# Kernel optimization log

Measured on AMD Instinct MI355X. Metric: run time of the kernel, lower is better.

Reference implementation:

```python
import jax, jax.numpy as jnp
import numpy as np

BS, N, D = 4, 512, 128

def setup_inputs() -> dict:
    key = jax.random.key(0)
    ks = jax.random.split(key, 8)
    s = 1.0 / np.sqrt(D)
    return {
        "x":  jax.random.normal(ks[0], (BS, N, D), dtype=jnp.float32),
        "Wq": jax.random.normal(ks[1], (D, D), dtype=jnp.float32) * s,
        "bq": jax.random.normal(ks[2], (D,), dtype=jnp.float32) * s,
        "Wk": jax.random.normal(ks[3], (D, D), dtype=jnp.float32) * s,
        "bk": jax.random.normal(ks[4], (D,), dtype=jnp.float32) * s,
        "Wv": jax.random.normal(ks[5], (D, D), dtype=jnp.float32) * s,
        "bv": jax.random.normal(ks[6], (D,), dtype=jnp.float32) * s,
        "pos_bias": jax.random.normal(ks[7], (N, N), dtype=jnp.float32) * 0.1,
    }

def reference(x, Wq, bq, Wk, bk, Wv, bv, pos_bias):
    # Linear projections (torch Linear: x @ W^T + b)
    q = jax.nn.sigmoid(jnp.einsum('bnd,ed->bne', x, Wq) + bq)   # [B,N,D]
    k = jnp.einsum('bnd,ed->bne', x, Wk) + bk                   # [B,N,D]
    v = jnp.einsum('bnd,ed->bne', x, Wv) + bv                   # [B,N,D]
    # scores[b,t,j,d] = k[b,j,d] + pos_bias[t,j]  (O(n^2 d) intermediate)
    s = k[:, None, :, :] + pos_bias[None, :, :, None]           # [B,N,N,D]
    m = jnp.max(s, axis=2, keepdims=True)                       # stabilizer
    e = jnp.exp(s - m)                                          # [B,N,N,D]
    num = jnp.einsum('btjd,bjd->btd', e, v)                     # [B,N,D]
    den = jnp.sum(e, axis=2)                                    # [B,N,D]
    return q * (num / den)
```

## Files before the change

### kernel.cpp

```cpp
#include <hip/hip_runtime.h>

#define BATCH 4
#define SEQ   512
#define DIM   128

typedef _Float16 half8 __attribute__((ext_vector_type(8)));
typedef _Float16 half4 __attribute__((ext_vector_type(4)));
typedef float    f32x4 __attribute__((ext_vector_type(4)));

__global__ __launch_bounds__(256) void k_prep(
    const float* __restrict__ x, const float* __restrict__ pos,
    const float* __restrict__ Wq, const float* __restrict__ Wk,
    const float* __restrict__ Wv,
    _Float16* __restrict__ x_h, _Float16* __restrict__ ep_h,
    _Float16* __restrict__ wq_h, _Float16* __restrict__ wk_h,
    _Float16* __restrict__ wv_h)
{
    const int blk = blockIdx.x;
    const int tid = threadIdx.x;
    if (blk < 128) {
        const int i = (blk * 256 + tid) * 8;
        const float4 p0 = *(const float4*)(x + i);
        const float4 p1 = *(const float4*)(x + i + 4);
        half8 h;
        h[0]=(_Float16)p0.x; h[1]=(_Float16)p0.y; h[2]=(_Float16)p0.z; h[3]=(_Float16)p0.w;
        h[4]=(_Float16)p1.x; h[5]=(_Float16)p1.y; h[6]=(_Float16)p1.z; h[7]=(_Float16)p1.w;
        *(half8*)(x_h + i) = h;
    } else if (blk < 256) {
        const int i = ((blk - 128) * 256 + tid) * 8;
        const float4 p0 = *(const float4*)(pos + i);
        const float4 p1 = *(const float4*)(pos + i + 4);
        half8 h;
        h[0]=(_Float16)__expf(p0.x); h[1]=(_Float16)__expf(p0.y);
        h[2]=(_Float16)__expf(p0.z); h[3]=(_Float16)__expf(p0.w);
        h[4]=(_Float16)__expf(p1.x); h[5]=(_Float16)__expf(p1.y);
        h[6]=(_Float16)__expf(p1.z); h[7]=(_Float16)__expf(p1.w);
        *(half8*)(ep_h + i) = h;
    } else {
        const int r = blk - 256;
        const float* src = (r < 8) ? Wq : ((r < 16) ? Wk : Wv);
        _Float16* dst    = (r < 8) ? wq_h : ((r < 16) ? wk_h : wv_h);
        const int i = ((r & 7) * 256 + tid) * 8;
        const float4 p0 = *(const float4*)(src + i);
        const float4 p1 = *(const float4*)(src + i + 4);
        half8 h;
        h[0]=(_Float16)p0.x; h[1]=(_Float16)p0.y; h[2]=(_Float16)p0.z; h[3]=(_Float16)p0.w;
        h[4]=(_Float16)p1.x; h[5]=(_Float16)p1.y; h[6]=(_Float16)p1.z; h[7]=(_Float16)p1.w;
        *(half8*)(dst + i) = h;
    }
}

__global__ __launch_bounds__(256) void k_proj(
    const _Float16* __restrict__ x_h,
    const _Float16* __restrict__ wq_h, const float* __restrict__ bq,
    const _Float16* __restrict__ wk_h, const float* __restrict__ bk,
    const _Float16* __restrict__ wv_h, const float* __restrict__ bv,
    float* __restrict__ qout, _Float16* __restrict__ ekk)
{
    const int tid  = threadIdx.x;
    const int lane = tid & 63;
    const int wave = tid >> 6;
    const int l15  = lane & 15;
    const int quad = lane >> 4;

    const int n0 = (blockIdx.x & 7) * 16;
    const int m0 = (blockIdx.x >> 3) * 64 + wave * 16;

    const _Float16* xa = x_h  + (m0 + l15) * DIM + quad * 8;
    const _Float16* wq = wq_h + (n0 + l15) * DIM + quad * 8;
    const _Float16* wk = wk_h + (n0 + l15) * DIM + quad * 8;
    const _Float16* wv = wv_h + (n0 + l15) * DIM + quad * 8;

    f32x4 aq = {0.f, 0.f, 0.f, 0.f};
    f32x4 ak = {0.f, 0.f, 0.f, 0.f};
    f32x4 av = {0.f, 0.f, 0.f, 0.f};

#pragma unroll
    for (int ks = 0; ks < 4; ++ks) {
        const half8 a  = *(const half8*)(xa + ks * 32);
        const half8 b0 = *(const half8*)(wq + ks * 32);
        const half8 b1 = *(const half8*)(wk + ks * 32);
        const half8 b2 = *(const half8*)(wv + ks * 32);
        aq = __builtin_amdgcn_mfma_f32_16x16x32_f16(a, b0, aq, 0, 0, 0);
        ak = __builtin_amdgcn_mfma_f32_16x16x32_f16(a, b1, ak, 0, 0, 0);
        av = __builtin_amdgcn_mfma_f32_16x16x32_f16(a, b2, av, 0, 0, 0);
    }

    const int c   = n0 + l15;
    const float bqv = bq[c];
    const float bkv = bk[c];
    const float bvv = bv[c];

    const int mrow = m0 + quad * 4;
    const int b    = mrow >> 9;
    const int tok  = mrow & 511;

    half4 eh, evh;
#pragma unroll
    for (int r = 0; r < 4; ++r) {
        const float e  = __expf(ak[r] + bkv);
        const float vv = av[r] + bvv;
        const float qv = 1.f / (1.f + __expf(-(aq[r] + bqv)));
        eh[r]  = (_Float16)e;
        evh[r] = (_Float16)(e * vv);
        qout[(b * SEQ + tok + r) * DIM + c] = qv;
    }
    *(half4*)(ekk + ((b * 256) + 2 * c + 0) * SEQ + tok) = eh;
    *(half4*)(ekk + ((b * 256) + 2 * c + 1) * SEQ + tok) = evh;
}

__global__ __launch_bounds__(256) void k_aft(
    const _Float16* __restrict__ ekk,
    const _Float16* __restrict__ ep_h,
    const float* __restrict__ qout,
    float* __restrict__ out)
{
    const int tid  = threadIdx.x;
    const int lane = tid & 63;
    const int wave = tid >> 6;
    const int l15  = lane & 15;
    const int quad = lane >> 4;
    const int wm   = wave & 1;
    const int wn   = wave >> 1;

    const int b  = blockIdx.x >> 6;
    const int m0 = (((blockIdx.x >> 3) & 7) * 32) + wm * 16;
    const int t0 = ((blockIdx.x & 7) * 64) + wn * 32;

    const _Float16* arow  = ekk  + ((b * 256) + m0 + l15) * SEQ + quad * 8;
    const _Float16* brow0 = ep_h + (t0 + l15) * SEQ + quad * 8;
    const _Float16* brow1 = brow0 + 16 * SEQ;

    f32x4 acc0 = {0.f, 0.f, 0.f, 0.f};
    f32x4 acc1 = {0.f, 0.f, 0.f, 0.f};

#pragma unroll
    for (int ks = 0; ks < 16; ++ks) {
        const half8 a  = *(const half8*)(arow  + ks * 32);
        const half8 b0 = *(const half8*)(brow0 + ks * 32);
        const half8 b1 = *(const half8*)(brow1 + ks * 32);
        acc0 = __builtin_amdgcn_mfma_f32_16x16x32_f16(a, b0, acc0, 0, 0, 0);
        acc1 = __builtin_amdgcn_mfma_f32_16x16x32_f16(a, b1, acc1, 0, 0, 0);
    }

    const int d0 = (m0 + quad * 4) >> 1;
#pragma unroll
    for (int i = 0; i < 2; ++i) {
        const f32x4 acc = i ? acc1 : acc0;
        const int t = t0 + i * 16 + l15;
        const float2 qv = *(const float2*)(qout + ((b * SEQ) + t) * DIM + d0);
        float2 o;
        o.x = qv.x * acc[1] / acc[0];
        o.y = qv.y * acc[3] / acc[2];
        *(float2*)(out + ((b * SEQ) + t) * DIM + d0) = o;
    }
}

extern "C" void kernel_launch(void* const* d_in, const int* in_sizes, int n_in,
                              void* d_out, int out_size, void* d_ws, size_t ws_size,
                              hipStream_t stream) {
    const float* x   = (const float*)d_in[0];
    const float* Wq  = (const float*)d_in[1];
    const float* bq  = (const float*)d_in[2];
    const float* Wk  = (const float*)d_in[3];
    const float* bk  = (const float*)d_in[4];
    const float* Wv  = (const float*)d_in[5];
    const float* bv  = (const float*)d_in[6];
    const float* pos = (const float*)d_in[7];

    float* outp = (float*)d_out;
    char*  ws   = (char*)d_ws;

    _Float16* x_h  = (_Float16*)(ws);
    _Float16* ep_h = (_Float16*)(ws + (512 << 10));
    _Float16* ekk  = (_Float16*)(ws + (1024 << 10));
    _Float16* wq_h = (_Float16*)(ws + (2048 << 10));
    _Float16* wk_h = (_Float16*)(ws + (2080 << 10));
    _Float16* wv_h = (_Float16*)(ws + (2112 << 10));
    float*    qout = (float*)   (ws + (2144 << 10));

    k_prep<<<280, 256, 0, stream>>>(x, pos, Wq, Wk, Wv, x_h, ep_h, wq_h, wk_h, wv_h);
    k_proj<<<256, 256, 0, stream>>>(x_h, wq_h, bq, wk_h, bk, wv_h, bv, qout, ekk);
    k_aft<<<256, 256, 0, stream>>>(ekk, ep_h, qout, outp);
}
```

Baseline: 79.88 us.

## Fold fp16 prep into projection kernel and spread AFT tiles over more waves

Removes the separate conversion kernel. The projection kernel now converts fp32 x and weights to fp16 in registers and also computes exp(pos_bias) into fp16. The q output is stored transposed as float4 per column. The AFT kernel uses 512-thread blocks with one 16x16 MFMA tile per wave instead of two, to raise parallelism. This saves one launch and an intermediate round trip, but each projection block re-reads and re-converts fp32 weights redundantly, and the q reads in the final epilogue become strided.

```diff
diff --git a/kernel.cpp b/kernel.cpp
--- a/kernel.cpp
+++ b/kernel.cpp
@@ -8,54 +8,21 @@
 typedef _Float16 half4 __attribute__((ext_vector_type(4)));
 typedef float    f32x4 __attribute__((ext_vector_type(4)));
 
-__global__ __launch_bounds__(256) void k_prep(
-    const float* __restrict__ x, const float* __restrict__ pos,
-    const float* __restrict__ Wq, const float* __restrict__ Wk,
-    const float* __restrict__ Wv,
-    _Float16* __restrict__ x_h, _Float16* __restrict__ ep_h,
-    _Float16* __restrict__ wq_h, _Float16* __restrict__ wk_h,
-    _Float16* __restrict__ wv_h)
-{
-    const int blk = blockIdx.x;
-    const int tid = threadIdx.x;
-    if (blk < 128) {
-        const int i = (blk * 256 + tid) * 8;
-        const float4 p0 = *(const float4*)(x + i);
-        const float4 p1 = *(const float4*)(x + i + 4);
-        half8 h;
-        h[0]=(_Float16)p0.x; h[1]=(_Float16)p0.y; h[2]=(_Float16)p0.z; h[3]=(_Float16)p0.w;
-        h[4]=(_Float16)p1.x; h[5]=(_Float16)p1.y; h[6]=(_Float16)p1.z; h[7]=(_Float16)p1.w;
-        *(half8*)(x_h + i) = h;
-    } else if (blk < 256) {
-        const int i = ((blk - 128) * 256 + tid) * 8;
-        const float4 p0 = *(const float4*)(pos + i);
-        const float4 p1 = *(const float4*)(pos + i + 4);
-        half8 h;
-        h[0]=(_Float16)__expf(p0.x); h[1]=(_Float16)__expf(p0.y);
-        h[2]=(_Float16)__expf(p0.z); h[3]=(_Float16)__expf(p0.w);
-        h[4]=(_Float16)__expf(p1.x); h[5]=(_Float16)__expf(p1.y);
-        h[6]=(_Float16)__expf(p1.z); h[7]=(_Float16)__expf(p1.w);
-        *(half8*)(ep_h + i) = h;
-    } else {
-        const int r = blk - 256;
-        const float* src = (r < 8) ? Wq : ((r < 16) ? Wk : Wv);
-        _Float16* dst    = (r < 8) ? wq_h : ((r < 16) ? wk_h : wv_h);
-        const int i = ((r & 7) * 256 + tid) * 8;
-        const float4 p0 = *(const float4*)(src + i);
-        const float4 p1 = *(const float4*)(src + i + 4);
-        half8 h;
-        h[0]=(_Float16)p0.x; h[1]=(_Float16)p0.y; h[2]=(_Float16)p0.z; h[3]=(_Float16)p0.w;
-        h[4]=(_Float16)p1.x; h[5]=(_Float16)p1.y; h[6]=(_Float16)p1.z; h[7]=(_Float16)p1.w;
-        *(half8*)(dst + i) = h;
-    }
+static __device__ __forceinline__ half8 cvt_h8(const float4 a, const float4 b) {
+    half8 h;
+    h[0] = (_Float16)a.x; h[1] = (_Float16)a.y; h[2] = (_Float16)a.z; h[3] = (_Float16)a.w;
+    h[4] = (_Float16)b.x; h[5] = (_Float16)b.y; h[6] = (_Float16)b.z; h[7] = (_Float16)b.w;
+    return h;
 }
 
 __global__ __launch_bounds__(256) void k_proj(
-    const _Float16* __restrict__ x_h,
-    const _Float16* __restrict__ wq_h, const float* __restrict__ bq,
-    const _Float16* __restrict__ wk_h, const float* __restrict__ bk,
-    const _Float16* __restrict__ wv_h, const float* __restrict__ bv,
-    float* __restrict__ qout, _Float16* __restrict__ ekk)
+    const float* __restrict__ x,
+    const float* __restrict__ Wq, const float* __restrict__ bq,
+    const float* __restrict__ Wk, const float* __restrict__ bk,
+    const float* __restrict__ Wv, const float* __restrict__ bv,
+    const float* __restrict__ pos,
+    float* __restrict__ qoutT, _Float16* __restrict__ ekk,
+    _Float16* __restrict__ ep_h)
 {
     const int tid  = threadIdx.x;
     const int lane = tid & 63;
@@ -66,10 +33,10 @@
     const int n0 = (blockIdx.x & 7) * 16;
     const int m0 = (blockIdx.x >> 3) * 64 + wave * 16;
 
-    const _Float16* xa = x_h  + (m0 + l15) * DIM + quad * 8;
-    const _Float16* wq = wq_h + (n0 + l15) * DIM + quad * 8;
-    const _Float16* wk = wk_h + (n0 + l15) * DIM + quad * 8;
-    const _Float16* wv = wv_h + (n0 + l15) * DIM + quad * 8;
+    const float* xa = x  + (m0 + l15) * DIM + quad * 8;
+    const float* wq = Wq + (n0 + l15) * DIM + quad * 8;
+    const float* wk = Wk + (n0 + l15) * DIM + quad * 8;
+    const float* wv = Wv + (n0 + l15) * DIM + quad * 8;
 
     f32x4 aq = {0.f, 0.f, 0.f, 0.f};
     f32x4 ak = {0.f, 0.f, 0.f, 0.f};
@@ -77,10 +44,14 @@
 
 #pragma unroll
     for (int ks = 0; ks < 4; ++ks) {
-        const half8 a  = *(const half8*)(xa + ks * 32);
-        const half8 b0 = *(const half8*)(wq + ks * 32);
-        const half8 b1 = *(const half8*)(wk + ks * 32);
-        const half8 b2 = *(const half8*)(wv + ks * 32);
+        const half8 a  = cvt_h8(*(const float4*)(xa + ks * 32),
+                                *(const float4*)(xa + ks * 32 + 4));
+        const half8 b0 = cvt_h8(*(const float4*)(wq + ks * 32),
+                                *(const float4*)(wq + ks * 32 + 4));
+        const half8 b1 = cvt_h8(*(const float4*)(wk + ks * 32),
+                                *(const float4*)(wk + ks * 32 + 4));
+        const half8 b2 = cvt_h8(*(const float4*)(wv + ks * 32),
+                                *(const float4*)(wv + ks * 32 + 4));
         aq = __builtin_amdgcn_mfma_f32_16x16x32_f16(a, b0, aq, 0, 0, 0);
         ak = __builtin_amdgcn_mfma_f32_16x16x32_f16(a, b1, ak, 0, 0, 0);
         av = __builtin_amdgcn_mfma_f32_16x16x32_f16(a, b2, av, 0, 0, 0);
@@ -96,23 +67,31 @@
     const int tok  = mrow & 511;
 
     half4 eh, evh;
+    float4 q4;
 #pragma unroll
     for (int r = 0; r < 4; ++r) {
         const float e  = __expf(ak[r] + bkv);
         const float vv = av[r] + bvv;
-        const float qv = 1.f / (1.f + __expf(-(aq[r] + bqv)));
         eh[r]  = (_Float16)e;
         evh[r] = (_Float16)(e * vv);
-        qout[(b * SEQ + tok + r) * DIM + c] = qv;
+        ((float*)&q4)[r] = 1.f / (1.f + __expf(-(aq[r] + bqv)));
     }
     *(half4*)(ekk + ((b * 256) + 2 * c + 0) * SEQ + tok) = eh;
     *(half4*)(ekk + ((b * 256) + 2 * c + 1) * SEQ + tok) = evh;
+    *(float4*)(qoutT + ((b * DIM) + c) * SEQ + tok) = q4;
+
+    const int i = (blockIdx.x * 256 + tid) * 4;
+    const float4 p = *(const float4*)(pos + i);
+    half4 h;
+    h[0] = (_Float16)__expf(p.x); h[1] = (_Float16)__expf(p.y);
+    h[2] = (_Float16)__expf(p.z); h[3] = (_Float16)__expf(p.w);
+    *(half4*)(ep_h + i) = h;
 }
 
-__global__ __launch_bounds__(256) void k_aft(
+__global__ __launch_bounds__(512, 2) void k_aft(
     const _Float16* __restrict__ ekk,
     const _Float16* __restrict__ ep_h,
-    const float* __restrict__ qout,
+    const float* __restrict__ qoutT,
     float* __restrict__ out)
 {
     const int tid  = threadIdx.x;
@@ -125,35 +104,28 @@
 
     const int b  = blockIdx.x >> 6;
     const int m0 = (((blockIdx.x >> 3) & 7) * 32) + wm * 16;
-    const int t0 = ((blockIdx.x & 7) * 64) + wn * 32;
+    const int t0 = ((blockIdx.x & 7) * 64) + wn * 16;
 
-    const _Float16* arow  = ekk  + ((b * 256) + m0 + l15) * SEQ + quad * 8;
-    const _Float16* brow0 = ep_h + (t0 + l15) * SEQ + quad * 8;
-    const _Float16* brow1 = brow0 + 16 * SEQ;
+    const _Float16* arow = ekk  + ((b * 256) + m0 + l15) * SEQ + quad * 8;
+    const _Float16* brow = ep_h + (t0 + l15) * SEQ + quad * 8;
 
-    f32x4 acc0 = {0.f, 0.f, 0.f, 0.f};
-    f32x4 acc1 = {0.f, 0.f, 0.f, 0.f};
+    f32x4 acc = {0.f, 0.f, 0.f, 0.f};
 
 #pragma unroll
     for (int ks = 0; ks < 16; ++ks) {
-        const half8 a  = *(const half8*)(arow  + ks * 32);
-        const half8 b0 = *(const half8*)(brow0 + ks * 32);
-        const half8 b1 = *(const half8*)(brow1 + ks * 32);
-        acc0 = __builtin_amdgcn_mfma_f32_16x16x32_f16(a, b0, acc0, 0, 0, 0);
-        acc1 = __builtin_amdgcn_mfma_f32_16x16x32_f16(a, b1, acc1, 0, 0, 0);
+        const half8 a  = *(const half8*)(arow + ks * 32);
+        const half8 bf = *(const half8*)(brow + ks * 32);
+        acc = __builtin_amdgcn_mfma_f32_16x16x32_f16(a, bf, acc, 0, 0, 0);
     }
 
     const int d0 = (m0 + quad * 4) >> 1;
-#pragma unroll
-    for (int i = 0; i < 2; ++i) {
-        const f32x4 acc = i ? acc1 : acc0;
-        const int t = t0 + i * 16 + l15;
-        const float2 qv = *(const float2*)(qout + ((b * SEQ) + t) * DIM + d0);
-        float2 o;
-        o.x = qv.x * acc[1] / acc[0];
-        o.y = qv.y * acc[3] / acc[2];
-        *(float2*)(out + ((b * SEQ) + t) * DIM + d0) = o;
-    }
+    const int t  = t0 + l15;
+    const float q0 = qoutT[((b * DIM) + d0) * SEQ + t];
+    const float q1 = qoutT[((b * DIM) + d0 + 1) * SEQ + t];
+    float2 o;
+    o.x = q0 * acc[1] / acc[0];
+    o.y = q1 * acc[3] / acc[2];
+    *(float2*)(out + ((b * SEQ) + t) * DIM + d0) = o;
 }
 
 extern "C" void kernel_launch(void* const* d_in, const int* in_sizes, int n_in,
@@ -171,15 +143,10 @@
     float* outp = (float*)d_out;
     char*  ws   = (char*)d_ws;
 
-    _Float16* x_h  = (_Float16*)(ws);
-    _Float16* ep_h = (_Float16*)(ws + (512 << 10));
-    _Float16* ekk  = (_Float16*)(ws + (1024 << 10));
-    _Float16* wq_h = (_Float16*)(ws + (2048 << 10));
-    _Float16* wk_h = (_Float16*)(ws + (2080 << 10));
-    _Float16* wv_h = (_Float16*)(ws + (2112 << 10));
-    float*    qout = (float*)   (ws + (2144 << 10));
+    _Float16* ep_h  = (_Float16*)(ws);
+    _Float16* ekk   = (_Float16*)(ws + (512 << 10));
+    float*    qoutT = (float*)   (ws + (1536 << 10));
 
-    k_prep<<<280, 256, 0, stream>>>(x, pos, Wq, Wk, Wv, x_h, ep_h, wq_h, wk_h, wv_h);
-    k_proj<<<256, 256, 0, stream>>>(x_h, wq_h, bq, wk_h, bk, wv_h, bv, qout, ekk);
-    k_aft<<<256, 256, 0, stream>>>(ekk, ep_h, qout, outp);
+    k_proj<<<256, 256, 0, stream>>>(x, Wq, bq, Wk, bk, Wv, bv, pos, qoutT, ekk, ep_h);
+    k_aft <<<256, 512, 0, stream>>>(ekk, ep_h, qoutT, outp);
 }
```

Result: no change. 80.91 us (+1.3%).
